# Performance work log

Measured on AMD Instinct MI355X. Metric: run time of the kernel, lower is better.

## Reference

```python
import jax, jax.numpy as jnp
import numpy as np

B, L, D = 16384, 50, 32  # batch, history length, embedding_dim
NU, NI, NC = 100000, 100000, 1000


def setup_inputs() -> dict:
    key = jax.random.key(0)
    ks = jax.random.split(key, 16)
    customer_id = jax.random.randint(ks[0], (B,), 0, NU)
    candidate_good = jax.random.randint(ks[1], (B,), 0, NI)
    candidate_class = jax.random.randint(ks[2], (B,), 0, NC)
    history_goods = jax.random.randint(ks[3], (B, L), 0, NI)
    history_classes = jax.random.randint(ks[4], (B, L), 0, NC)
    user_table = jax.random.normal(ks[5], (NU, D), jnp.float32) * 0.05
    item_table = jax.random.normal(ks[6], (NI, D), jnp.float32) * 0.05
    item_table = item_table.at[0].set(0.0)  # padding_idx=0
    cat_table = jax.random.normal(ks[7], (NC, D), jnp.float32) * 0.05
    cat_table = cat_table.at[0].set(0.0)  # padding_idx=0
    # attention net: Linear(4*2D=256 -> 80), Linear(80 -> 1)
    aw1 = jax.random.normal(ks[8], (4 * 2 * D, 80), jnp.float32) * 0.05
    ab1 = jnp.zeros((80,), jnp.float32)
    aw2 = jax.random.normal(ks[9], (80, 1), jnp.float32) * 0.05
    ab2 = jnp.zeros((1,), jnp.float32)
    # final mlp: 5D=160 -> 256 -> 128 -> 1
    mw1 = jax.random.normal(ks[10], (5 * D, 256), jnp.float32) * 0.05
    mb1 = jnp.zeros((256,), jnp.float32)
    mw2 = jax.random.normal(ks[11], (256, 128), jnp.float32) * 0.05
    mb2 = jnp.zeros((128,), jnp.float32)
    mw3 = jax.random.normal(ks[12], (128, 1), jnp.float32) * 0.05
    mb3 = jnp.zeros((1,), jnp.float32)
    return dict(customer_id=customer_id, candidate_good=candidate_good,
                candidate_class=candidate_class, history_goods=history_goods,
                history_classes=history_classes, user_table=user_table,
                item_table=item_table, cat_table=cat_table,
                aw1=aw1, ab1=ab1, aw2=aw2, ab2=ab2,
                mw1=mw1, mb1=mb1, mw2=mw2, mb2=mb2, mw3=mw3, mb3=mb3)


def reference(customer_id, candidate_good, candidate_class, history_goods,
              history_classes, user_table, item_table, cat_table,
              aw1, ab1, aw2, ab2, mw1, mb1, mw2, mb2, mw3, mb3):
    user_emb = user_table[customer_id]                               # [B, D]
    cand = jnp.concatenate([item_table[candidate_good],
                            cat_table[candidate_class]], axis=-1)    # [B, 2D]
    hist = jnp.concatenate([item_table[history_goods],
                            cat_table[history_classes]], axis=-1)    # [B, L, 2D]
    q = jnp.broadcast_to(cand[:, None, :], hist.shape)               # [B, L, 2D]
    info = jnp.concatenate([q, hist, q - hist, q * hist], axis=-1)   # [B, L, 8D]
    h = jax.nn.relu(info @ aw1 + ab1)                                # [B, L, 80]
    scores = (h @ aw2 + ab2)[..., 0]                                 # [B, L]
    mask = history_goods != 0
    scores = jnp.where(mask, scores, -1e9)
    weights = jax.nn.softmax(scores, axis=1)                         # [B, L]
    att = jnp.einsum('bl,bld->bd', weights, hist)                    # [B, 2D]
    combined = jnp.concatenate([user_emb, cand, att], axis=-1)       # [B, 5D]
    z = jax.nn.relu(combined @ mw1 + mb1)
    z = jax.nn.relu(z @ mw2 + mb2)
    out = (z @ mw3 + mb3)[..., 0]                                    # [B]
    return out
```

## Files before the change

kernel.cpp:

```cpp
#include <hip/hip_runtime.h>
#include <hip/hip_bf16.h>
#include <math.h>

#define LHIST 50

typedef __attribute__((ext_vector_type(8))) short bf16x8;
typedef __attribute__((ext_vector_type(4))) float f32x4;

__device__ __forceinline__ unsigned short f2bf(float f) {
    union { float f; unsigned u; } v; v.f = f;
    unsigned r = v.u + 0x7fff + ((v.u >> 16) & 1);
    return (unsigned short)(r >> 16);
}
__device__ __forceinline__ float bf2f(unsigned short h) {
    union { unsigned u; float f; } v; v.u = ((unsigned)h) << 16;
    return v.f;
}
__device__ __forceinline__ unsigned pk2(float lo, float hi) {
    __hip_bfloat162 h = __float22bfloat162_rn(make_float2(lo, hi));
    return *(unsigned*)&h;
}
__device__ __forceinline__ float bflo(unsigned u){ union{unsigned v;float f;} x; x.v = u << 16; return x.f; }
__device__ __forceinline__ float bfhi(unsigned u){ union{unsigned v;float f;} x; x.v = u & 0xffff0000u; return x.f; }


__global__ void prep_kernel(const float* __restrict__ aw1,
                            const float* __restrict__ mw1,
                            const float* __restrict__ mw2,
                            const float* __restrict__ item_table,
                            const float* __restrict__ cat_table,
                            int itemN, int catN,
                            float* __restrict__ Awt,
                            unsigned short* __restrict__ Bmfb,
                            unsigned short* __restrict__ W4fb,
                            unsigned short* __restrict__ W1f,
                            unsigned short* __restrict__ W2f,
                            unsigned short* __restrict__ itemb,
                            unsigned short* __restrict__ catb) {
    int i = blockIdx.x * 256 + threadIdx.x;
    int i8 = i * 8;
    if (i8 + 7 < itemN) {
        float4 a = *(const float4*)&item_table[i8];
        float4 b = *(const float4*)&item_table[i8 + 4];
        uint4 r;
        r.x = pk2(a.x, a.y); r.y = pk2(a.z, a.w);
        r.z = pk2(b.x, b.y); r.w = pk2(b.z, b.w);
        *(uint4*)&itemb[i8] = r;
    }
    if (i8 + 7 < catN) {
        float4 a = *(const float4*)&cat_table[i8];
        float4 b = *(const float4*)&cat_table[i8 + 4];
        uint4 r;
        r.x = pk2(a.x, a.y); r.y = pk2(a.z, a.w);
        r.z = pk2(b.x, b.y); r.w = pk2(b.z, b.w);
        *(uint4*)&catb[i8] = r;
    }
    if (i < 5120) {
        int j = i >> 6, k = i & 63;
        Awt[i] = aw1[k * 80 + j] + aw1[(128 + k) * 80 + j];
        int kk = i / 80, n = i - kk * 80;
        int nt = n >> 4, colw = n & 15, ks = kk >> 5, r = kk & 31, qd = r >> 3, off = r & 7;
        int d = ((nt * 2 + ks) * 64 + qd * 16 + colw) * 8 + off;
        Bmfb[d] = f2bf(aw1[(64 + kk) * 80 + n] - aw1[(128 + kk) * 80 + n]);
        W4fb[d] = f2bf(aw1[(192 + kk) * 80 + n]);
    }
    if (i < 40960) {
        int kk = i >> 8, n = i & 255;
        int nt = n >> 4, colw = n & 15, ks = kk >> 5, r = kk & 31, qd = r >> 3, off = r & 7;
        W1f[((nt * 5 + ks) * 64 + qd * 16 + colw) * 8 + off] = f2bf(mw1[i]);
    }
    if (i < 32768) {
        int kk = i >> 7, n = i & 127;
        int nt = n >> 4, colw = n & 15, ks = kk >> 5, r = kk & 31, qd = r >> 3, off = r & 7;
        W2f[((nt * 8 + ks) * 64 + qd * 16 + colw) * 8 + off] = f2bf(mw2[i]);
    }
}

__global__ void __launch_bounds__(256, 6) attn_kernel(
    const int* __restrict__ cid, const int* __restrict__ cg,
    const int* __restrict__ cc,  const int* __restrict__ hg,
    const int* __restrict__ hc,
    const float* __restrict__ user_table, const float* __restrict__ item_table,
    const float* __restrict__ cat_table,
    const float* __restrict__ ab1, const float* __restrict__ aw2,
    const float* __restrict__ Awt, const unsigned short* __restrict__ Bmfb,
    const unsigned short* __restrict__ W4fb,
    const unsigned short* __restrict__ itemb, const unsigned short* __restrict__ catb,
    float* __restrict__ combined)
{
    __shared__ __align__(16) unsigned short sh_Bq[2][5120];
    __shared__ __align__(16) float sh_q[2][64];
    __shared__ float sh_bias[2][80];
    __shared__ float sh_sc[2][64];
    __shared__ float sh_aw2[80];
    __shared__ float sh_att[4][64];

    const int t = threadIdx.x;
    const int b0 = blockIdx.x * 2;
    const int wv = t >> 6;
    const int lane = t & 63;
    const int quad = lane >> 4;
    const int col = lane & 15;
    const int bb = wv >> 1;
    const int hwv = wv & 1;
    const int b = b0 + bb;

    int il[2], ic[2];
    #pragma unroll
    for (int mi = 0; mi < 2; ++mi) {
        int l = hwv * 32 + mi * 16 + col;
        int lc = (l < LHIST) ? l : 0;
        il[mi] = hg[b * LHIST + lc];
        ic[mi] = hc[b * LHIST + lc];
    }
    uint4 vi[2], vc[2];
    #pragma unroll
    for (int mi = 0; mi < 2; ++mi) {
        vi[mi] = *(const uint4*)&itemb[(size_t)il[mi] * 32 + quad * 8];
        vc[mi] = *(const uint4*)&catb[(size_t)ic[mi] * 32 + quad * 8];
    }
    if (t < 128) {
        int qbi = t >> 6, k = t & 63;
        int bq = b0 + qbi;
        float v = (k < 32) ? item_table[(size_t)cg[bq] * 32 + k]
                           : cat_table[(size_t)cc[bq] * 32 + (k - 32)];
        sh_q[qbi][k] = v;
    }
    if (t < 80) sh_aw2[t] = aw2[t];
    __syncthreads();

    for (int slot = t; slot < 640; slot += 256) {
        int j = slot * 8;
        int lane8 = slot & 63, ks = (slot >> 6) & 1;
        int kk = ks * 32 + (lane8 >> 4) * 8;
        uint4 bm4 = *(const uint4*)&Bmfb[j];
        uint4 w44 = *(const uint4*)&W4fb[j];
        unsigned bw[4] = {bm4.x, bm4.y, bm4.z, bm4.w};
        unsigned ww[4] = {w44.x, w44.y, w44.z, w44.w};
        float bl[8], wl4[8];
        #pragma unroll
        for (int d = 0; d < 4; ++d) {
            bl[2 * d] = bflo(bw[d]);  bl[2 * d + 1] = bfhi(bw[d]);
            wl4[2 * d] = bflo(ww[d]); wl4[2 * d + 1] = bfhi(ww[d]);
        }
        #pragma unroll
        for (int bb2 = 0; bb2 < 2; ++bb2) {
            float4 qa = *(const float4*)&sh_q[bb2][kk];
            float4 qb = *(const float4*)&sh_q[bb2][kk + 4];
            float qv[8] = {qa.x, qa.y, qa.z, qa.w, qb.x, qb.y, qb.z, qb.w};
            uint4 res;
            unsigned* rp = (unsigned*)&res;
            #pragma unroll
            for (int d = 0; d < 4; ++d)
                rp[d] = pk2(bl[2 * d]     + qv[2 * d]     * wl4[2 * d],
                            bl[2 * d + 1] + qv[2 * d + 1] * wl4[2 * d + 1]);
            *(uint4*)&sh_Bq[bb2][j] = res;
        }
    }
    if (t < 160) {
        int bi = t >= 80;
        int j = t - bi * 80;
        float acc = ab1[j];
        const float4* aw = (const float4*)&Awt[j * 64];
        #pragma unroll
        for (int k4 = 0; k4 < 16; ++k4) {
            float4 a = aw[k4];
            float4 q = *(const float4*)&sh_q[bi][k4 * 4];
            acc += a.x * q.x + a.y * q.y + a.z * q.z + a.w * q.w;
        }
        sh_bias[bi][j] = acc;
    }
    __syncthreads();

    float4 a2v[5], bv[5];
    #pragma unroll
    for (int jt = 0; jt < 5; ++jt) {
        a2v[jt] = *(const float4*)&sh_aw2[jt * 16 + quad * 4];
        bv[jt]  = *(const float4*)&sh_bias[bb][jt * 16 + quad * 4];
    }

    bf16x8 hi0 = *(bf16x8*)&vi[0];
    bf16x8 hc0 = *(bf16x8*)&vc[0];
    bf16x8 hi1 = *(bf16x8*)&vi[1];
    bf16x8 hc1 = *(bf16x8*)&vc[1];
    float px = 0.f, py = 0.f;
    #pragma unroll
    for (int jt = 0; jt < 5; ++jt) {
        f32x4 a0 = (f32x4){0.f, 0.f, 0.f, 0.f};
        f32x4 a1 = (f32x4){0.f, 0.f, 0.f, 0.f};
        bf16x8 A0 = *(const bf16x8*)&sh_Bq[bb][((jt * 2 + 0) * 64 + lane) * 8];
        bf16x8 A1 = *(const bf16x8*)&sh_Bq[bb][((jt * 2 + 1) * 64 + lane) * 8];
        a0 = __builtin_amdgcn_mfma_f32_16x16x32_bf16(A0, hi0, a0, 0, 0, 0);
        a0 = __builtin_amdgcn_mfma_f32_16x16x32_bf16(A1, hc0, a0, 0, 0, 0);
        a1 = __builtin_amdgcn_mfma_f32_16x16x32_bf16(A0, hi1, a1, 0, 0, 0);
        a1 = __builtin_amdgcn_mfma_f32_16x16x32_bf16(A1, hc1, a1, 0, 0, 0);
        const float* bp = (const float*)&bv[jt];
        const float* ap = (const float*)&a2v[jt];
        #pragma unroll
        for (int i = 0; i < 4; ++i) {
            px += fmaxf(a0[i] + bp[i], 0.f) * ap[i];
            py += fmaxf(a1[i] + bp[i], 0.f) * ap[i];
        }
    }
    px += __shfl_xor(px, 16); px += __shfl_xor(px, 32);
    py += __shfl_xor(py, 16); py += __shfl_xor(py, 32);
    if (quad == 0) {
        sh_sc[bb][hwv * 32 + col] = px;
        sh_sc[bb][hwv * 32 + 16 + col] = py;
    }
    __syncthreads();

    float sc = -INFINITY;
    if (lane < LHIST) {
        sc = sh_sc[bb][lane];
        if (hg[b * LHIST + lane] == 0) sc = -1e9f;
    }
    float m = sc;
    #pragma unroll
    for (int off = 32; off > 0; off >>= 1) m = fmaxf(m, __shfl_xor(m, off));
    float e = (lane < LHIST) ? __expf(sc - m) : 0.f;
    float ssum = e;
    #pragma unroll
    for (int off = 32; off > 0; off >>= 1) ssum += __shfl_xor(ssum, off);
    float w = e / ssum;

    {
        float wl0 = __shfl(w, hwv * 32 + col);
        float wl1 = __shfl(w, hwv * 32 + 16 + col);
        union { uint4 u; unsigned short s[8]; } i0, i1, c0u, c1u;
        i0.u = vi[0]; i1.u = vi[1]; c0u.u = vc[0]; c1u.u = vc[1];
        float ati[8], atc[8];
        #pragma unroll
        for (int j = 0; j < 8; ++j) {
            ati[j] = wl0 * bf2f(i0.s[j]) + wl1 * bf2f(i1.s[j]);
            atc[j] = wl0 * bf2f(c0u.s[j]) + wl1 * bf2f(c1u.s[j]);
        }
        float* red = (float*)sh_Bq;
        float* myrow = red + wv * 1056 + col * 66;
        #pragma unroll
        for (int j2 = 0; j2 < 4; ++j2) {
            *(float2*)&myrow[quad * 8 + j2 * 2]      = make_float2(ati[2 * j2], ati[2 * j2 + 1]);
            *(float2*)&myrow[33 + quad * 8 + j2 * 2] = make_float2(atc[2 * j2], atc[2 * j2 + 1]);
        }
        int colIdx = (lane < 32) ? lane : 33 + (lane - 32);
        float s = 0.f;
        #pragma unroll
        for (int c = 0; c < 16; ++c) s += red[wv * 1056 + c * 66 + colIdx];
        sh_att[wv][lane] = s;
    }
    __syncthreads();

    if (wv < 2) {
        int bo = b0 + wv;
        float* crow = combined + (size_t)bo * 160;
        crow[32 + lane] = sh_q[wv][lane];
        crow[96 + lane] = sh_att[2 * wv][lane] + sh_att[2 * wv + 1][lane];
        if (lane < 32) crow[lane] = user_table[(size_t)cid[bo] * 32 + lane];
    }
}

__global__ void __launch_bounds__(256, 4) mlp_kernel(
    const float* __restrict__ combined,
    const unsigned short* __restrict__ W1f, const unsigned short* __restrict__ W2f,
    const float* __restrict__ mb1, const float* __restrict__ mb2,
    const float* __restrict__ mw3, const float* __restrict__ mb3,
    float* __restrict__ out)
{
    __shared__ __align__(16) unsigned short shA1[5120];
    __shared__ __align__(16) unsigned short shA2[8192];
    __shared__ float sh_part[4][32];

    const int t = threadIdx.x;
    const int b0 = blockIdx.x * 32;
    const int wv = t >> 6;
    const int lane = t & 63;
    const int quad = lane >> 4;
    const int col = lane & 15;

    for (int i = t; i < 1280; i += 256) {
        int m = i / 40;
        int s = i - m * 40;
        int k0 = s * 4;
        float4 v = *(const float4*)&combined[(size_t)(b0 + m) * 160 + k0];
        int mt = m >> 4, colm = m & 15;
        int ks = k0 >> 5, qd = (k0 >> 3) & 3, off = k0 & 7;
        ushort4 r; r.x = f2bf(v.x); r.y = f2bf(v.y); r.z = f2bf(v.z); r.w = f2bf(v.w);
        *(ushort4*)&shA1[((mt * 5 + ks) * 64 + qd * 16 + colm) * 8 + off] = r;
    }
    __syncthreads();

    f32x4 acc1[2][4];
    #pragma unroll
    for (int mt = 0; mt < 2; ++mt)
        #pragma unroll
        for (int j = 0; j < 4; ++j) acc1[mt][j] = (f32x4){0.f, 0.f, 0.f, 0.f};
    #pragma unroll
    for (int ks = 0; ks < 5; ++ks) {
        bf16x8 a0 = *(const bf16x8*)&shA1[(ks * 64 + lane) * 8];
        bf16x8 a1 = *(const bf16x8*)&shA1[((5 + ks) * 64 + lane) * 8];
        #pragma unroll
        for (int j = 0; j < 4; ++j) {
            int ntg = wv * 4 + j;
            bf16x8 bw = *(const bf16x8*)&W1f[((ntg * 5 + ks) * 64 + lane) * 8];
            acc1[0][j] = __builtin_amdgcn_mfma_f32_16x16x32_bf16(a0, bw, acc1[0][j], 0, 0, 0);
            acc1[1][j] = __builtin_amdgcn_mfma_f32_16x16x32_bf16(a1, bw, acc1[1][j], 0, 0, 0);
        }
    }
    #pragma unroll
    for (int j = 0; j < 4; ++j) {
        int n = (wv * 4 + j) * 16 + col;
        float bj = mb1[n];
        int ks2 = n >> 5, qd2 = (n >> 3) & 3, off2 = n & 7;
        #pragma unroll
        for (int mt = 0; mt < 2; ++mt)
            #pragma unroll
            for (int i = 0; i < 4; ++i) {
                float z = fmaxf(acc1[mt][j][i] + bj, 0.f);
                shA2[((mt * 8 + ks2) * 64 + qd2 * 16 + quad * 4 + i) * 8 + off2] = f2bf(z);
            }
    }
    __syncthreads();

    f32x4 acc2[2][2];
    #pragma unroll
    for (int mt = 0; mt < 2; ++mt)
        #pragma unroll
        for (int jj = 0; jj < 2; ++jj) acc2[mt][jj] = (f32x4){0.f, 0.f, 0.f, 0.f};
    #pragma unroll
    for (int ks = 0; ks < 8; ++ks) {
        bf16x8 a0 = *(const bf16x8*)&shA2[(ks * 64 + lane) * 8];
        bf16x8 a1 = *(const bf16x8*)&shA2[((8 + ks) * 64 + lane) * 8];
        #pragma unroll
        for (int jj = 0; jj < 2; ++jj) {
            int ntg = wv * 2 + jj;
            bf16x8 bw = *(const bf16x8*)&W2f[((ntg * 8 + ks) * 64 + lane) * 8];
            acc2[0][jj] = __builtin_amdgcn_mfma_f32_16x16x32_bf16(a0, bw, acc2[0][jj], 0, 0, 0);
            acc2[1][jj] = __builtin_amdgcn_mfma_f32_16x16x32_bf16(a1, bw, acc2[1][jj], 0, 0, 0);
        }
    }
    #pragma unroll
    for (int mt = 0; mt < 2; ++mt) {
        #pragma unroll
        for (int i = 0; i < 4; ++i) {
            float p = 0.f;
            #pragma unroll
            for (int jj = 0; jj < 2; ++jj) {
                int n = (wv * 2 + jj) * 16 + col;
                float z = fmaxf(acc2[mt][jj][i] + mb2[n], 0.f);
                p += z * mw3[n];
            }
            p += __shfl_xor(p, 1);
            p += __shfl_xor(p, 2);
            p += __shfl_xor(p, 4);
            p += __shfl_xor(p, 8);
            if (col == 0) sh_part[wv][mt * 16 + quad * 4 + i] = p;
        }
    }
    __syncthreads();
    if (t < 32)
        out[b0 + t] = sh_part[0][t] + sh_part[1][t] + sh_part[2][t] + sh_part[3][t] + mb3[0];
}

extern "C" void kernel_launch(void* const* d_in, const int* in_sizes, int n_in,
                              void* d_out, int out_size, void* d_ws, size_t ws_size,
                              hipStream_t stream) {
    const int*   cid = (const int*)d_in[0];
    const int*   cg  = (const int*)d_in[1];
    const int*   cc  = (const int*)d_in[2];
    const int*   hg  = (const int*)d_in[3];
    const int*   hc  = (const int*)d_in[4];
    const float* user_table = (const float*)d_in[5];
    const float* item_table = (const float*)d_in[6];
    const float* cat_table  = (const float*)d_in[7];
    const float* aw1 = (const float*)d_in[8];
    const float* ab1 = (const float*)d_in[9];
    const float* aw2 = (const float*)d_in[10];
    const float* mw1 = (const float*)d_in[12];
    const float* mb1 = (const float*)d_in[13];
    const float* mw2 = (const float*)d_in[14];
    const float* mb2 = (const float*)d_in[15];
    const float* mw3 = (const float*)d_in[16];
    const float* mb3 = (const float*)d_in[17];
    float* out = (float*)d_out;

    const int B = in_sizes[0];
    const int itemN = in_sizes[6];
    const int catN  = in_sizes[7];
    float* ws = (float*)d_ws;
    float* Awt = ws;
    unsigned short* Bmfb = (unsigned short*)(ws + 5120);
    unsigned short* W4fb = (unsigned short*)(ws + 7680);
    unsigned short* W1f  = (unsigned short*)(ws + 10240);
    unsigned short* W2f  = (unsigned short*)(ws + 30720);
    unsigned short* itemb = (unsigned short*)(ws + 47104);
    unsigned short* catb  = itemb + itemN;
    float* combined = ws + 47104 + (itemN + catN + 1) / 2;

    int n8 = (itemN + 7) / 8;
    int prep_grid = (n8 + 255) / 256;
    if (prep_grid < 160) prep_grid = 160;
    prep_kernel<<<prep_grid, 256, 0, stream>>>(aw1, mw1, mw2, item_table, cat_table,
                                               itemN, catN, Awt, Bmfb, W4fb, W1f, W2f,
                                               itemb, catb);
    attn_kernel<<<B / 2, 256, 0, stream>>>(cid, cg, cc, hg, hc,
                                           user_table, item_table, cat_table,
                                           ab1, aw2, Awt, Bmfb, W4fb, itemb, catb, combined);
    mlp_kernel<<<B / 32, 256, 0, stream>>>(combined, W1f, W2f,
                                           mb1, mb2, mw3, mb3, out);
}
```

Measured before the change: 189.4 us.

## Compute attention per wave with shared weights, MFMA bias, q*hist operand

The attention kernel now gives each wave one batch row, so a block covers four rows, and block-wide syncs are no longer needed. The old version built a per-row weight matrix combining q into shared memory. The new version uses the fixed bf16 weight fragments straight from global memory, puts q*hist into the B operand, and computes the query bias term with MFMA using a new combined W1+W3 fragment. Softmax and the weighted sum now run within a single wave. The trade-off is twice as many MFMAs per row, extra bf16 rounding of q*hist, and lower declared occupancy (launch bounds 4 instead of 6).

Result: slower. 341.9 us (+80.5%).

```diff
diff --git a/kernel.cpp b/kernel.cpp
--- a/kernel.cpp
+++ b/kernel.cpp
@@ -20,8 +20,6 @@
     __hip_bfloat162 h = __float22bfloat162_rn(make_float2(lo, hi));
     return *(unsigned*)&h;
 }
-__device__ __forceinline__ float bflo(unsigned u){ union{unsigned v;float f;} x; x.v = u << 16; return x.f; }
-__device__ __forceinline__ float bfhi(unsigned u){ union{unsigned v;float f;} x; x.v = u & 0xffff0000u; return x.f; }
 
 
 __global__ void prep_kernel(const float* __restrict__ aw1,
@@ -30,7 +28,7 @@
                             const float* __restrict__ item_table,
                             const float* __restrict__ cat_table,
                             int itemN, int catN,
-                            float* __restrict__ Awt,
+                            unsigned short* __restrict__ W13fb,
                             unsigned short* __restrict__ Bmfb,
                             unsigned short* __restrict__ W4fb,
                             unsigned short* __restrict__ W1f,
@@ -56,13 +54,12 @@
         *(uint4*)&catb[i8] = r;
     }
     if (i < 5120) {
-        int j = i >> 6, k = i & 63;
-        Awt[i] = aw1[k * 80 + j] + aw1[(128 + k) * 80 + j];
         int kk = i / 80, n = i - kk * 80;
         int nt = n >> 4, colw = n & 15, ks = kk >> 5, r = kk & 31, qd = r >> 3, off = r & 7;
         int d = ((nt * 2 + ks) * 64 + qd * 16 + colw) * 8 + off;
-        Bmfb[d] = f2bf(aw1[(64 + kk) * 80 + n] - aw1[(128 + kk) * 80 + n]);
-        W4fb[d] = f2bf(aw1[(192 + kk) * 80 + n]);
+        Bmfb[d]  = f2bf(aw1[(64 + kk) * 80 + n] - aw1[(128 + kk) * 80 + n]);
+        W4fb[d]  = f2bf(aw1[(192 + kk) * 80 + n]);
+        W13fb[d] = f2bf(aw1[kk * 80 + n] + aw1[(128 + kk) * 80 + n]);
     }
     if (i < 40960) {
         int kk = i >> 8, n = i & 255;
@@ -76,187 +73,172 @@
     }
 }
 
-__global__ void __launch_bounds__(256, 6) attn_kernel(
+__global__ void __launch_bounds__(256, 4) attn_kernel(
     const int* __restrict__ cid, const int* __restrict__ cg,
     const int* __restrict__ cc,  const int* __restrict__ hg,
     const int* __restrict__ hc,
     const float* __restrict__ user_table, const float* __restrict__ item_table,
     const float* __restrict__ cat_table,
     const float* __restrict__ ab1, const float* __restrict__ aw2,
-    const float* __restrict__ Awt, const unsigned short* __restrict__ Bmfb,
+    const unsigned short* __restrict__ W13fb, const unsigned short* __restrict__ Bmfb,
     const unsigned short* __restrict__ W4fb,
     const unsigned short* __restrict__ itemb, const unsigned short* __restrict__ catb,
     float* __restrict__ combined)
 {
-    __shared__ __align__(16) unsigned short sh_Bq[2][5120];
-    __shared__ __align__(16) float sh_q[2][64];
-    __shared__ float sh_bias[2][80];
-    __shared__ float sh_sc[2][64];
-    __shared__ float sh_aw2[80];
-    __shared__ float sh_att[4][64];
+    __shared__ float red[4][1056];
 
     const int t = threadIdx.x;
-    const int b0 = blockIdx.x * 2;
     const int wv = t >> 6;
     const int lane = t & 63;
     const int quad = lane >> 4;
     const int col = lane & 15;
-    const int bb = wv >> 1;
-    const int hwv = wv & 1;
-    const int b = b0 + bb;
-
-    int il[2], ic[2];
-    #pragma unroll
-    for (int mi = 0; mi < 2; ++mi) {
-        int l = hwv * 32 + mi * 16 + col;
+    const int b = blockIdx.x * 4 + wv;
+
+    const int cgb = cg[b], ccb = cc[b];
+
+    int il[4], ic[4];
+    bool bad[4];
+    #pragma unroll
+    for (int mi = 0; mi < 4; ++mi) {
+        int l = mi * 16 + col;
         int lc = (l < LHIST) ? l : 0;
         il[mi] = hg[b * LHIST + lc];
         ic[mi] = hc[b * LHIST + lc];
-    }
-    uint4 vi[2], vc[2];
-    #pragma unroll
-    for (int mi = 0; mi < 2; ++mi) {
+        bad[mi] = (l >= LHIST) || (il[mi] == 0);
+    }
+    uint4 vi[4], vc[4];
+    #pragma unroll
+    for (int mi = 0; mi < 4; ++mi) {
         vi[mi] = *(const uint4*)&itemb[(size_t)il[mi] * 32 + quad * 8];
         vc[mi] = *(const uint4*)&catb[(size_t)ic[mi] * 32 + quad * 8];
     }
-    if (t < 128) {
-        int qbi = t >> 6, k = t & 63;
-        int bq = b0 + qbi;
-        float v = (k < 32) ? item_table[(size_t)cg[bq] * 32 + k]
-                           : cat_table[(size_t)cc[bq] * 32 + (k - 32)];
-        sh_q[qbi][k] = v;
-    }
-    if (t < 80) sh_aw2[t] = aw2[t];
-    __syncthreads();
-
-    for (int slot = t; slot < 640; slot += 256) {
-        int j = slot * 8;
-        int lane8 = slot & 63, ks = (slot >> 6) & 1;
-        int kk = ks * 32 + (lane8 >> 4) * 8;
-        uint4 bm4 = *(const uint4*)&Bmfb[j];
-        uint4 w44 = *(const uint4*)&W4fb[j];
-        unsigned bw[4] = {bm4.x, bm4.y, bm4.z, bm4.w};
-        unsigned ww[4] = {w44.x, w44.y, w44.z, w44.w};
-        float bl[8], wl4[8];
-        #pragma unroll
-        for (int d = 0; d < 4; ++d) {
-            bl[2 * d] = bflo(bw[d]);  bl[2 * d + 1] = bfhi(bw[d]);
-            wl4[2 * d] = bflo(ww[d]); wl4[2 * d + 1] = bfhi(ww[d]);
-        }
-        #pragma unroll
-        for (int bb2 = 0; bb2 < 2; ++bb2) {
-            float4 qa = *(const float4*)&sh_q[bb2][kk];
-            float4 qb = *(const float4*)&sh_q[bb2][kk + 4];
-            float qv[8] = {qa.x, qa.y, qa.z, qa.w, qb.x, qb.y, qb.z, qb.w};
-            uint4 res;
-            unsigned* rp = (unsigned*)&res;
-            #pragma unroll
-            for (int d = 0; d < 4; ++d)
-                rp[d] = pk2(bl[2 * d]     + qv[2 * d]     * wl4[2 * d],
-                            bl[2 * d + 1] + qv[2 * d + 1] * wl4[2 * d + 1]);
-            *(uint4*)&sh_Bq[bb2][j] = res;
-        }
-    }
-    if (t < 160) {
-        int bi = t >= 80;
-        int j = t - bi * 80;
-        float acc = ab1[j];
-        const float4* aw = (const float4*)&Awt[j * 64];
-        #pragma unroll
-        for (int k4 = 0; k4 < 16; ++k4) {
-            float4 a = aw[k4];
-            float4 q = *(const float4*)&sh_q[bi][k4 * 4];
-            acc += a.x * q.x + a.y * q.y + a.z * q.z + a.w * q.w;
-        }
-        sh_bias[bi][j] = acc;
-    }
-    __syncthreads();
-
-    float4 a2v[5], bv[5];
+    const float4 qia = *(const float4*)&item_table[(size_t)cgb * 32 + quad * 8];
+    const float4 qib = *(const float4*)&item_table[(size_t)cgb * 32 + quad * 8 + 4];
+    const float4 qca = *(const float4*)&cat_table[(size_t)ccb * 32 + quad * 8];
+    const float4 qcb = *(const float4*)&cat_table[(size_t)ccb * 32 + quad * 8 + 4];
+
+    bf16x8 qbi, qbc;
+    {
+        uint4 u, v;
+        u.x = pk2(qia.x, qia.y); u.y = pk2(qia.z, qia.w);
+        u.z = pk2(qib.x, qib.y); u.w = pk2(qib.z, qib.w);
+        v.x = pk2(qca.x, qca.y); v.y = pk2(qca.z, qca.w);
+        v.z = pk2(qcb.x, qcb.y); v.w = pk2(qcb.z, qcb.w);
+        qbi = *(bf16x8*)&u;
+        qbc = *(bf16x8*)&v;
+    }
+
+    bf16x8 hqi[4], hqc[4];
+    #pragma unroll
+    for (int mi = 0; mi < 4; ++mi) {
+        union { uint4 u; unsigned short s[8]; } h;
+        h.u = vi[mi];
+        uint4 r;
+        r.x = pk2(bf2f(h.s[0]) * qia.x, bf2f(h.s[1]) * qia.y);
+        r.y = pk2(bf2f(h.s[2]) * qia.z, bf2f(h.s[3]) * qia.w);
+        r.z = pk2(bf2f(h.s[4]) * qib.x, bf2f(h.s[5]) * qib.y);
+        r.w = pk2(bf2f(h.s[6]) * qib.z, bf2f(h.s[7]) * qib.w);
+        hqi[mi] = *(bf16x8*)&r;
+        h.u = vc[mi];
+        uint4 rc;
+        rc.x = pk2(bf2f(h.s[0]) * qca.x, bf2f(h.s[1]) * qca.y);
+        rc.y = pk2(bf2f(h.s[2]) * qca.z, bf2f(h.s[3]) * qca.w);
+        rc.z = pk2(bf2f(h.s[4]) * qcb.x, bf2f(h.s[5]) * qcb.y);
+        rc.w = pk2(bf2f(h.s[6]) * qcb.z, bf2f(h.s[7]) * qcb.w);
+        hqc[mi] = *(bf16x8*)&rc;
+    }
+
+    f32x4 accb[5];
     #pragma unroll
     for (int jt = 0; jt < 5; ++jt) {
-        a2v[jt] = *(const float4*)&sh_aw2[jt * 16 + quad * 4];
-        bv[jt]  = *(const float4*)&sh_bias[bb][jt * 16 + quad * 4];
-    }
-
-    bf16x8 hi0 = *(bf16x8*)&vi[0];
-    bf16x8 hc0 = *(bf16x8*)&vc[0];
-    bf16x8 hi1 = *(bf16x8*)&vi[1];
-    bf16x8 hc1 = *(bf16x8*)&vc[1];
-    float px = 0.f, py = 0.f;
+        bf16x8 w0 = *(const bf16x8*)&W13fb[((jt * 2 + 0) * 64 + lane) * 8];
+        bf16x8 w1 = *(const bf16x8*)&W13fb[((jt * 2 + 1) * 64 + lane) * 8];
+        f32x4 a = (f32x4){0.f, 0.f, 0.f, 0.f};
+        a = __builtin_amdgcn_mfma_f32_16x16x32_bf16(w0, qbi, a, 0, 0, 0);
+        a = __builtin_amdgcn_mfma_f32_16x16x32_bf16(w1, qbc, a, 0, 0, 0);
+        float4 b4 = *(const float4*)&ab1[jt * 16 + quad * 4];
+        a[0] += b4.x; a[1] += b4.y; a[2] += b4.z; a[3] += b4.w;
+        accb[jt] = a;
+    }
+
+    float px[4] = {0.f, 0.f, 0.f, 0.f};
     #pragma unroll
     for (int jt = 0; jt < 5; ++jt) {
-        f32x4 a0 = (f32x4){0.f, 0.f, 0.f, 0.f};
-        f32x4 a1 = (f32x4){0.f, 0.f, 0.f, 0.f};
-        bf16x8 A0 = *(const bf16x8*)&sh_Bq[bb][((jt * 2 + 0) * 64 + lane) * 8];
-        bf16x8 A1 = *(const bf16x8*)&sh_Bq[bb][((jt * 2 + 1) * 64 + lane) * 8];
-        a0 = __builtin_amdgcn_mfma_f32_16x16x32_bf16(A0, hi0, a0, 0, 0, 0);
-        a0 = __builtin_amdgcn_mfma_f32_16x16x32_bf16(A1, hc0, a0, 0, 0, 0);
-        a1 = __builtin_amdgcn_mfma_f32_16x16x32_bf16(A0, hi1, a1, 0, 0, 0);
-        a1 = __builtin_amdgcn_mfma_f32_16x16x32_bf16(A1, hc1, a1, 0, 0, 0);
-        const float* bp = (const float*)&bv[jt];
-        const float* ap = (const float*)&a2v[jt];
-        #pragma unroll
-        for (int i = 0; i < 4; ++i) {
-            px += fmaxf(a0[i] + bp[i], 0.f) * ap[i];
-            py += fmaxf(a1[i] + bp[i], 0.f) * ap[i];
-        }
-    }
-    px += __shfl_xor(px, 16); px += __shfl_xor(px, 32);
-    py += __shfl_xor(py, 16); py += __shfl_xor(py, 32);
-    if (quad == 0) {
-        sh_sc[bb][hwv * 32 + col] = px;
-        sh_sc[bb][hwv * 32 + 16 + col] = py;
-    }
-    __syncthreads();
-
-    float sc = -INFINITY;
-    if (lane < LHIST) {
-        sc = sh_sc[bb][lane];
-        if (hg[b * LHIST + lane] == 0) sc = -1e9f;
-    }
-    float m = sc;
-    #pragma unroll
-    for (int off = 32; off > 0; off >>= 1) m = fmaxf(m, __shfl_xor(m, off));
-    float e = (lane < LHIST) ? __expf(sc - m) : 0.f;
-    float ssum = e;
-    #pragma unroll
-    for (int off = 32; off > 0; off >>= 1) ssum += __shfl_xor(ssum, off);
-    float w = e / ssum;
-
-    {
-        float wl0 = __shfl(w, hwv * 32 + col);
-        float wl1 = __shfl(w, hwv * 32 + 16 + col);
-        union { uint4 u; unsigned short s[8]; } i0, i1, c0u, c1u;
-        i0.u = vi[0]; i1.u = vi[1]; c0u.u = vc[0]; c1u.u = vc[1];
-        float ati[8], atc[8];
+        bf16x8 a23_0 = *(const bf16x8*)&Bmfb[((jt * 2 + 0) * 64 + lane) * 8];
+        bf16x8 a23_1 = *(const bf16x8*)&Bmfb[((jt * 2 + 1) * 64 + lane) * 8];
+        bf16x8 a4_0  = *(const bf16x8*)&W4fb[((jt * 2 + 0) * 64 + lane) * 8];
+        bf16x8 a4_1  = *(const bf16x8*)&W4fb[((jt * 2 + 1) * 64 + lane) * 8];
+        float4 a2 = *(const float4*)&aw2[jt * 16 + quad * 4];
+        #pragma unroll
+        for (int mi = 0; mi < 4; ++mi) {
+            f32x4 acc = accb[jt];
+            acc = __builtin_amdgcn_mfma_f32_16x16x32_bf16(a23_0, *(bf16x8*)&vi[mi], acc, 0, 0, 0);
+            acc = __builtin_amdgcn_mfma_f32_16x16x32_bf16(a23_1, *(bf16x8*)&vc[mi], acc, 0, 0, 0);
+            acc = __builtin_amdgcn_mfma_f32_16x16x32_bf16(a4_0, hqi[mi], acc, 0, 0, 0);
+            acc = __builtin_amdgcn_mfma_f32_16x16x32_bf16(a4_1, hqc[mi], acc, 0, 0, 0);
+            px[mi] += fmaxf(acc[0], 0.f) * a2.x
+                    + fmaxf(acc[1], 0.f) * a2.y
+                    + fmaxf(acc[2], 0.f) * a2.z
+                    + fmaxf(acc[3], 0.f) * a2.w;
+        }
+    }
+
+    #pragma unroll
+    for (int mi = 0; mi < 4; ++mi) {
+        px[mi] += __shfl_xor(px[mi], 16);
+        px[mi] += __shfl_xor(px[mi], 32);
+    }
+
+    float sc[4];
+    #pragma unroll
+    for (int mi = 0; mi < 4; ++mi) sc[mi] = bad[mi] ? -1e9f : px[mi];
+    float m = fmaxf(fmaxf(sc[0], sc[1]), fmaxf(sc[2], sc[3]));
+    #pragma unroll
+    for (int off = 8; off >= 1; off >>= 1) m = fmaxf(m, __shfl_xor(m, off));
+    float e[4];
+    float ssum = 0.f;
+    #pragma unroll
+    for (int mi = 0; mi < 4; ++mi) {
+        int l = mi * 16 + col;
+        e[mi] = (l < LHIST) ? __expf(sc[mi] - m) : 0.f;
+        ssum += e[mi];
+    }
+    #pragma unroll
+    for (int off = 8; off >= 1; off >>= 1) ssum += __shfl_xor(ssum, off);
+    float inv = 1.f / ssum;
+
+    float ati[8], atc[8];
+    #pragma unroll
+    for (int j = 0; j < 8; ++j) { ati[j] = 0.f; atc[j] = 0.f; }
+    #pragma unroll
+    for (int mi = 0; mi < 4; ++mi) {
+        float w = e[mi] * inv;
+        union { uint4 u; unsigned short s[8]; } hi_, hc_;
+        hi_.u = vi[mi]; hc_.u = vc[mi];
         #pragma unroll
         for (int j = 0; j < 8; ++j) {
-            ati[j] = wl0 * bf2f(i0.s[j]) + wl1 * bf2f(i1.s[j]);
-            atc[j] = wl0 * bf2f(c0u.s[j]) + wl1 * bf2f(c1u.s[j]);
-        }
-        float* red = (float*)sh_Bq;
-        float* myrow = red + wv * 1056 + col * 66;
-        #pragma unroll
-        for (int j2 = 0; j2 < 4; ++j2) {
-            *(float2*)&myrow[quad * 8 + j2 * 2]      = make_float2(ati[2 * j2], ati[2 * j2 + 1]);
-            *(float2*)&myrow[33 + quad * 8 + j2 * 2] = make_float2(atc[2 * j2], atc[2 * j2 + 1]);
-        }
-        int colIdx = (lane < 32) ? lane : 33 + (lane - 32);
-        float s = 0.f;
-        #pragma unroll
-        for (int c = 0; c < 16; ++c) s += red[wv * 1056 + c * 66 + colIdx];
-        sh_att[wv][lane] = s;
-    }
-    __syncthreads();
-
-    if (wv < 2) {
-        int bo = b0 + wv;
-        float* crow = combined + (size_t)bo * 160;
-        crow[32 + lane] = sh_q[wv][lane];
-        crow[96 + lane] = sh_att[2 * wv][lane] + sh_att[2 * wv + 1][lane];
-        if (lane < 32) crow[lane] = user_table[(size_t)cid[bo] * 32 + lane];
-    }
+            ati[j] += w * bf2f(hi_.s[j]);
+            atc[j] += w * bf2f(hc_.s[j]);
+        }
+    }
+
+    float* myrow = &red[wv][col * 66];
+    #pragma unroll
+    for (int j2 = 0; j2 < 4; ++j2) {
+        *(float2*)&myrow[quad * 8 + 2 * j2]      = make_float2(ati[2 * j2], ati[2 * j2 + 1]);
+        *(float2*)&myrow[33 + quad * 8 + 2 * j2] = make_float2(atc[2 * j2], atc[2 * j2 + 1]);
+    }
+    int colIdx = (lane < 32) ? lane : 33 + (lane - 32);
+    float s = 0.f;
+    #pragma unroll
+    for (int c = 0; c < 16; ++c) s += red[wv][c * 66 + colIdx];
+
+    float* crow = combined + (size_t)b * 160;
+    const int cidb = cid[b];
+    crow[lane] = (lane < 32) ? user_table[(size_t)cidb * 32 + lane]
+                             : item_table[(size_t)cgb * 32 + (lane - 32)];
+    if (lane < 32) crow[64 + lane] = cat_table[(size_t)ccb * 32 + lane];
+    crow[96 + lane] = s;
 }
 
 __global__ void __launch_bounds__(256, 4) mlp_kernel(
@@ -387,7 +369,7 @@
     const int itemN = in_sizes[6];
     const int catN  = in_sizes[7];
     float* ws = (float*)d_ws;
-    float* Awt = ws;
+    unsigned short* W13fb = (unsigned short*)ws;
     unsigned short* Bmfb = (unsigned short*)(ws + 5120);
     unsigned short* W4fb = (unsigned short*)(ws + 7680);
     unsigned short* W1f  = (unsigned short*)(ws + 10240);
@@ -400,11 +382,11 @@
     int prep_grid = (n8 + 255) / 256;
     if (prep_grid < 160) prep_grid = 160;
     prep_kernel<<<prep_grid, 256, 0, stream>>>(aw1, mw1, mw2, item_table, cat_table,
-                                               itemN, catN, Awt, Bmfb, W4fb, W1f, W2f,
+                                               itemN, catN, W13fb, Bmfb, W4fb, W1f, W2f,
                                                itemb, catb);
-    attn_kernel<<<B / 2, 256, 0, stream>>>(cid, cg, cc, hg, hc,
+    attn_kernel<<<B / 4, 256, 0, stream>>>(cid, cg, cc, hg, hc,
                                            user_table, item_table, cat_table,
-                                           ab1, aw2, Awt, Bmfb, W4fb, itemb, catb, combined);
+                                           ab1, aw2, W13fb, Bmfb, W4fb, itemb, catb, combined);
     mlp_kernel<<<B / 32, 256, 0, stream>>>(combined, W1f, W2f,
                                            mb1, mb2, mw3, mb3, out);
 }
```
